# Performance work log

Measured on AMD Instinct MI355X. Metric: run time of the kernel, lower is better.

## Reference

```python
import jax, jax.numpy as jnp
import numpy as np

BETA = 0.1
EPS_LOW = 0.2
EPS_HIGH = 0.2
TEMPERATURE = 1.0
H, V = 1024, 32000
B, T = 4, 1024


def _per_token_logps(hidden, weight, ids):
    # hidden: [B,T,H], weight: [V,H], ids: [B,T] -> gathered log-softmax logps [B,T]
    logits = jnp.einsum('bth,vh->btv', hidden, weight) / TEMPERATURE  # [B,T,V]
    lse = jax.nn.logsumexp(logits, axis=-1)                            # [B,T]
    sel = jnp.take_along_axis(logits, ids[..., None], axis=-1)[..., 0]
    return sel - lse


def setup_inputs() -> dict:
    key = jax.random.key(0)
    k1, k2, k3, k4, k5, k6 = jax.random.split(key, 6)
    x = jax.random.normal(k1, (B, T, H), dtype=jnp.float32)
    ref_input = jax.random.normal(k2, (B, T, H), dtype=jnp.float32)
    # lm-head weights (policy and frozen reference), scaled like nn.Linear init
    weight = jax.random.normal(k3, (V, H), dtype=jnp.float32) * (1.0 / np.sqrt(H))
    ref_weight = jax.random.normal(k4, (V, H), dtype=jnp.float32) * (1.0 / np.sqrt(H))
    selected_token_ids = jax.random.randint(k5, (B, T), 0, V, dtype=jnp.int32)
    attention_mask = jnp.ones((B, T), dtype=jnp.int32)
    advantages = jax.random.normal(k6, (B,), dtype=jnp.float32)
    return {
        'x': x,
        'weight': weight,
        'ref_input': ref_input,
        'ref_weight': ref_weight,
        'advantages': advantages,
        'selected_token_ids': selected_token_ids,
        'attention_mask': attention_mask,
    }


def reference(x, weight, ref_input, ref_weight, advantages, selected_token_ids, attention_mask):
    # policy per-token logps
    logps = _per_token_logps(x, weight, selected_token_ids)  # [B,T]
    # reference model logps (no grad path in original)
    ref_logps = jax.lax.stop_gradient(
        _per_token_logps(ref_input, ref_weight, selected_token_ids))
    # old logps default: detached current logps -> ratio = 1 in forward
    old_logps = jax.lax.stop_gradient(logps)

    log_ratio = logps - old_logps
    coef_1 = jnp.exp(log_ratio)
    coef_2 = jnp.clip(coef_1, 1.0 - EPS_LOW, 1.0 + EPS_HIGH)
    adv = advantages[:, None]  # [B,1]
    per_token_loss = -jnp.minimum(coef_1 * adv, coef_2 * adv)

    # KL penalty to reference model: exp(ref-cur) - (ref-cur) - 1
    d = ref_logps - logps
    kl = jnp.exp(d) - d - 1.0
    per_token_loss = per_token_loss + BETA * kl

    mask = attention_mask.astype(per_token_loss.dtype)
    # loss_type 'bnpo': batch-normalized policy optimization
    loss = jnp.sum(per_token_loss * mask) / jnp.maximum(jnp.sum(mask), 1.0)
    return loss
```

## Files before the change

kernel.cpp:

```cpp
#include <hip/hip_runtime.h>
#include <hip/hip_bf16.h>
#include <math.h>

constexpr int kH   = 1024;
constexpr int kV   = 32000;
constexpr int kTok = 4096;
constexpr int BM   = 256;
constexpr int BN   = 256;
constexpr int BK   = 64;
constexpr int NT   = kH / BK;
constexpr int NVT  = kV / BN;
constexpr int NMT  = kTok / BM;

typedef _Float16 f16x8  __attribute__((ext_vector_type(8)));
typedef float    f32x16 __attribute__((ext_vector_type(16)));

typedef __attribute__((address_space(1))) const void gvoid_t;
typedef __attribute__((address_space(3))) void lvoid_t;

__global__ __launch_bounds__(256) void convert_kernel(
    const float* __restrict__ src, _Float16* __restrict__ dst)
{
  int idx = blockIdx.x * 256 + threadIdx.x;
  int row = idx >> 7;
  int blk = idx & 127;
  int chunk = blk >> 3;
  int c = blk & 7;
  int p = c ^ (row & 7);
  const float* s = src + ((size_t)row << 10) + (blk << 3);
  float4 v0 = *(const float4*)s;
  float4 v1 = *(const float4*)(s + 4);
  f16x8 o = { (_Float16)v0.x, (_Float16)v0.y, (_Float16)v0.z, (_Float16)v0.w,
              (_Float16)v1.x, (_Float16)v1.y, (_Float16)v1.z, (_Float16)v1.w };
  *(f16x8*)&dst[((size_t)row << 10) + (chunk << 6) + (p << 3)] = o;
}

__global__ __launch_bounds__(512, 2) void lse_gemm_kernel(
    const _Float16* __restrict__ X0, const _Float16* __restrict__ W0,
    const _Float16* __restrict__ X1, const _Float16* __restrict__ W1,
    float2* __restrict__ P0, float2* __restrict__ P1)
{
  __shared__ _Float16 lds[2][2][BM * BK];

  const _Float16* Xp = blockIdx.z ? X1 : X0;
  const _Float16* Wp = blockIdx.z ? W1 : W0;
  float2* Pp = blockIdx.z ? P1 : P0;

  const int tid  = threadIdx.x;
  const int wave = tid >> 6;
  const int lane = tid & 63;
  const int l31  = lane & 31;
  const int h    = lane >> 5;
  const int ll7  = lane & 7;
  const int wr   = wave >> 2;
  const int wc   = wave & 3;
  const int srow = lane >> 3;
  const int sblk = lane & 7;

  const int m_base = blockIdx.x * BM;
  const int v_base = blockIdx.y * BN;

  const _Float16* gA = Xp + (size_t)(m_base + wave * 8 + srow) * kH + sblk * 8;
  const _Float16* gB = Wp + (size_t)(v_base + wave * 8 + srow) * kH + sblk * 8;

  const int baseA = (wr * 128 + l31) * BK;
  const int baseV = (wc * 64  + l31) * BK;
  int offK[4];
#pragma unroll
  for (int s = 0; s < 4; ++s) offK[s] = (((s * 2 + h) ^ ll7) << 3);

  f32x16 acc[2][4];
#pragma unroll
  for (int j = 0; j < 2; ++j)
#pragma unroll
    for (int i = 0; i < 4; ++i)
#pragma unroll
      for (int r = 0; r < 16; ++r) acc[j][i][r] = 0.f;

  f16x8 vf[2][4];
  f16x8 tfa[4], tfb[4];

#define STG_A(c, kt, hh) do {                                                       \
    __builtin_amdgcn_global_load_lds(                                               \
        (gvoid_t*)(gA + (size_t)((hh) * 128     ) * kH + (kt) * BK),                \
        (lvoid_t*)&lds[c][0][(((hh) * 128     ) + wave * 8) * BK], 16, 0, 0);       \
    __builtin_amdgcn_global_load_lds(                                               \
        (gvoid_t*)(gA + (size_t)((hh) * 128 + 64) * kH + (kt) * BK),                \
        (lvoid_t*)&lds[c][0][(((hh) * 128 + 64) + wave * 8) * BK], 16, 0, 0);       \
  } while (0)
#define STG_B(c, kt, hh) do {                                                       \
    __builtin_amdgcn_global_load_lds(                                               \
        (gvoid_t*)(gB + (size_t)((hh) * 128     ) * kH + (kt) * BK),                \
        (lvoid_t*)&lds[c][1][(((hh) * 128     ) + wave * 8) * BK], 16, 0, 0);       \
    __builtin_amdgcn_global_load_lds(                                               \
        (gvoid_t*)(gB + (size_t)((hh) * 128 + 64) * kH + (kt) * BK),                \
        (lvoid_t*)&lds[c][1][(((hh) * 128 + 64) + wave * 8) * BK], 16, 0, 0);       \
  } while (0)

#define BAR do { asm volatile("" ::: "memory");                                     \
                 __builtin_amdgcn_s_barrier();                                      \
                 asm volatile("" ::: "memory"); } while (0)
#define VM6  asm volatile("s_waitcnt vmcnt(6)" ::: "memory")
#define VM0  asm volatile("s_waitcnt vmcnt(0)" ::: "memory")

#define RDTF(dst, c, f) do {                                                        \
    _Pragma("unroll")                                                               \
    for (int s = 0; s < 4; ++s)                                                     \
      dst[s] = *(const f16x8*)&lds[c][0][baseA + (f) * 2048 + offK[s]];             \
  } while (0)
#define RDVF(c) do {                                                                \
    _Pragma("unroll")                                                               \
    for (int j = 0; j < 2; ++j)                                                     \
      _Pragma("unroll")                                                             \
      for (int s = 0; s < 4; ++s)                                                   \
        vf[j][s] = *(const f16x8*)&lds[c][1][baseV + j * 2048 + offK[s]];           \
  } while (0)

#define MM(g, TF) do {                                                              \
    __builtin_amdgcn_s_setprio(1);                                                  \
    _Pragma("unroll")                                                               \
    for (int s = 0; s < 4; ++s) {                                                   \
      acc[0][g] = __builtin_amdgcn_mfma_f32_32x32x16_f16(vf[0][s], TF[s], acc[0][g], 0, 0, 0); \
      acc[1][g] = __builtin_amdgcn_mfma_f32_32x32x16_f16(vf[1][s], TF[s], acc[1][g], 0, 0, 0); \
    }                                                                               \
    __builtin_amdgcn_s_setprio(0);                                                  \
  } while (0)

  STG_B(0, 0, 0); STG_B(0, 0, 1); STG_A(0, 0, 0); STG_A(0, 0, 1);
  STG_B(1, 1, 0); STG_B(1, 1, 1); STG_A(1, 1, 0);
  VM6;
  BAR;
  RDVF(0);
  RDTF(tfa, 0, 0);

  for (int kt = 0; kt < NT - 2; kt += 2) {
    STG_A(1, kt + 1, 1); BAR; RDTF(tfb, 0, 1); MM(0, tfa); BAR;
    STG_B(0, kt + 2, 0); BAR; RDTF(tfa, 0, 2); MM(1, tfb); BAR;
    STG_B(0, kt + 2, 1); BAR; RDTF(tfb, 0, 3); MM(2, tfa); BAR;
    STG_A(0, kt + 2, 0); VM6; BAR; RDTF(tfa, 1, 0); MM(3, tfb); RDVF(1); BAR;
    STG_A(0, kt + 2, 1); BAR; RDTF(tfb, 1, 1); MM(0, tfa); BAR;
    STG_B(1, kt + 3, 0); BAR; RDTF(tfa, 1, 2); MM(1, tfb); BAR;
    STG_B(1, kt + 3, 1); BAR; RDTF(tfb, 1, 3); MM(2, tfa); BAR;
    STG_A(1, kt + 3, 0); VM6; BAR; RDTF(tfa, 0, 0); MM(3, tfb); RDVF(0); BAR;
  }

  STG_A(1, NT - 1, 1); BAR; RDTF(tfb, 0, 1); MM(0, tfa); BAR;
  BAR;                      RDTF(tfa, 0, 2); MM(1, tfb); BAR;
  BAR;                      RDTF(tfb, 0, 3); MM(2, tfa); BAR;
  VM0; BAR;                 RDTF(tfa, 1, 0); MM(3, tfb); RDVF(1); BAR;
  BAR;                      RDTF(tfb, 1, 1); MM(0, tfa); BAR;
  BAR;                      RDTF(tfa, 1, 2); MM(1, tfb); BAR;
  BAR;                      RDTF(tfb, 1, 3); MM(2, tfa); BAR;
  BAR;                                       MM(3, tfb);

#undef STG_A
#undef STG_B
#undef RDTF
#undef RDVF
#undef MM

  float* redm = (float*)&lds[0][0][0];
  float* reds = redm + 4 * 256;

#pragma unroll
  for (int i = 0; i < 4; ++i) {
    float m = acc[0][i][0];
#pragma unroll
    for (int r = 1; r < 16; ++r) m = fmaxf(m, acc[0][i][r]);
#pragma unroll
    for (int r = 0; r < 16; ++r) m = fmaxf(m, acc[1][i][r]);
    float s = 0.f;
#pragma unroll
    for (int r = 0; r < 16; ++r) s += __expf(acc[0][i][r] - m);
#pragma unroll
    for (int r = 0; r < 16; ++r) s += __expf(acc[1][i][r] - m);
    float om = __shfl_xor(m, 32, 64);
    float os = __shfl_xor(s, 32, 64);
    float nm = fmaxf(m, om);
    s = s * __expf(m - nm) + os * __expf(om - nm);
    m = nm;
    if (lane < 32) {
      redm[wc * 256 + wr * 128 + i * 32 + lane] = m;
      reds[wc * 256 + wr * 128 + i * 32 + lane] = s;
    }
  }
  __syncthreads();
  if (tid < 256) {
    float M = redm[tid], S = reds[tid];
#pragma unroll
    for (int w = 1; w < 4; ++w) {
      float m2 = redm[w * 256 + tid], s2 = reds[w * 256 + tid];
      float nm = fmaxf(M, m2);
      S = S * __expf(M - nm) + s2 * __expf(m2 - nm);
      M = nm;
    }
    Pp[(size_t)blockIdx.y * kTok + m_base + tid] = make_float2(M, S);
  }
}

__global__ __launch_bounds__(256) void sel_kernel(
    const float* __restrict__ X0, const float* __restrict__ W0,
    const float* __restrict__ X1, const float* __restrict__ W1,
    const int* __restrict__ ids, float* __restrict__ sel0, float* __restrict__ sel1)
{
  const int model = blockIdx.y;
  const float* X = model ? X1 : X0;
  const float* W = model ? W1 : W0;
  float* out = model ? sel1 : sel0;
  const int wave = threadIdx.x >> 6, lane = threadIdx.x & 63;
  const int t  = blockIdx.x * 4 + wave;
  const int id = ids[t];
  const float* xr = X + (size_t)t * kH;
  const float* wr = W + (size_t)id * kH;
  float s = 0.f;
#pragma unroll
  for (int r = 0; r < 4; ++r) {
    int idx = r * 256 + lane * 4;
    float4 a = *(const float4*)&xr[idx];
    float4 b = *(const float4*)&wr[idx];
    s += a.x * b.x + a.y * b.y + a.z * b.z + a.w * b.w;
  }
#pragma unroll
  for (int st = 32; st; st >>= 1) s += __shfl_xor(s, st, 64);
  if (lane == 0) out[t] = s;
}

__global__ __launch_bounds__(256) void finalize_kernel(
    const float2* __restrict__ P0, const float2* __restrict__ P1,
    const float* __restrict__ sel0, const float* __restrict__ sel1,
    const float* __restrict__ adv, const int* __restrict__ mask,
    float* __restrict__ accum)
{
  const int t = blockIdx.x * 256 + threadIdx.x;
  float M0 = -INFINITY, S0 = 0.f, M1 = -INFINITY, S1 = 0.f;
  for (int i = 0; i < NVT; ++i) {
    float2 p = P0[(size_t)i * kTok + t];
    if (p.x > M0) { S0 = S0 * __expf(M0 - p.x) + p.y; M0 = p.x; }
    else          { S0 += p.y * __expf(p.x - M0); }
  }
  for (int i = 0; i < NVT; ++i) {
    float2 p = P1[(size_t)i * kTok + t];
    if (p.x > M1) { S1 = S1 * __expf(M1 - p.x) + p.y; M1 = p.x; }
    else          { S1 += p.y * __expf(p.x - M1); }
  }
  float lse0  = M0 + logf(S0);
  float lse1  = M1 + logf(S1);
  float logp  = sel0[t] - lse0;
  float rlogp = sel1[t] - lse1;
  float d  = rlogp - logp;
  float kl = __expf(d) - d - 1.f;
  float a  = adv[t >> 10];
  float mv = (float)mask[t];
  float loss = (-a + 0.1f * kl) * mv;

#pragma unroll
  for (int st = 32; st; st >>= 1) {
    loss += __shfl_xor(loss, st, 64);
    mv   += __shfl_xor(mv, st, 64);
  }
  __shared__ float lsum[4], msum[4];
  const int wave = threadIdx.x >> 6, lane = threadIdx.x & 63;
  if (lane == 0) { lsum[wave] = loss; msum[wave] = mv; }
  __syncthreads();
  if (threadIdx.x == 0) {
    atomicAdd(&accum[0], lsum[0] + lsum[1] + lsum[2] + lsum[3]);
    atomicAdd(&accum[1], msum[0] + msum[1] + msum[2] + msum[3]);
  }
}

__global__ void scalar_kernel(const float* __restrict__ accum, float* __restrict__ out)
{
  out[0] = accum[0] / fmaxf(accum[1], 1.f);
}

extern "C" void kernel_launch(void* const* d_in, const int* in_sizes, int n_in,
                              void* d_out, int out_size, void* d_ws, size_t ws_size,
                              hipStream_t stream)
{
  const float* x    = (const float*)d_in[0];
  const float* w    = (const float*)d_in[1];
  const float* rx   = (const float*)d_in[2];
  const float* rw   = (const float*)d_in[3];
  const float* adv  = (const float*)d_in[4];
  const int*   ids  = (const int*)d_in[5];
  const int*   mask = (const int*)d_in[6];
  float* out = (float*)d_out;

  char* ws = (char*)d_ws;
  _Float16* Xh  = (_Float16*)ws;
  _Float16* Wh  = Xh + (size_t)kTok * kH;
  _Float16* RXh = Wh + (size_t)kV * kH;
  _Float16* RWh = RXh + (size_t)kTok * kH;
  float2*   P0  = (float2*)(RWh + (size_t)kV * kH);
  float2*   P1  = P0 + (size_t)NVT * kTok;
  float*    sel0 = (float*)(P1 + (size_t)NVT * kTok);
  float*    sel1 = sel0 + kTok;
  float*    accum = sel1 + kTok;

  hipMemsetAsync(accum, 0, 2 * sizeof(float), stream);

  convert_kernel<<<kTok * 128 / 256, 256, 0, stream>>>(x,  Xh);
  convert_kernel<<<kV   * 128 / 256, 256, 0, stream>>>(w,  Wh);
  convert_kernel<<<kTok * 128 / 256, 256, 0, stream>>>(rx, RXh);
  convert_kernel<<<kV   * 128 / 256, 256, 0, stream>>>(rw, RWh);

  sel_kernel<<<dim3(kTok / 4, 2), 256, 0, stream>>>(x, w, rx, rw, ids, sel0, sel1);

  lse_gemm_kernel<<<dim3(NMT, NVT, 2), 512, 0, stream>>>(Xh, Wh, RXh, RWh, P0, P1);

  finalize_kernel<<<kTok / 256, 256, 0, stream>>>(P0, P1, sel0, sel1, adv, mask, accum);
  scalar_kernel<<<1, 1, 0, stream>>>(accum, out);
}
```

Baseline: 916.4 us.

## Pre-pack weights into MFMA fragment layout and load them directly to registers

The weight matrices are now converted into a layout already arranged as per-lane MFMA operand fragments, so the GEMM reads W straight from global memory into registers instead of staging it through LDS. LDS now holds only the X tile, which halves shared-memory use and the ds_read traffic, and the elaborate barrier-interleaved schedule is replaced by a simpler double-buffered loop with two syncthreads per pair of K steps. The cost is that W fragments go through L2/global loads per wave with no LDS reuse across waves in a block, and the coarser synchronisation offers less latency hiding.

```diff
diff --git a/kernel.cpp b/kernel.cpp
--- a/kernel.cpp
+++ b/kernel.cpp
@@ -18,7 +18,7 @@
 typedef __attribute__((address_space(1))) const void gvoid_t;
 typedef __attribute__((address_space(3))) void lvoid_t;
 
-__global__ __launch_bounds__(256) void convert_kernel(
+__global__ __launch_bounds__(256) void convert_x_kernel(
     const float* __restrict__ src, _Float16* __restrict__ dst)
 {
   int idx = blockIdx.x * 256 + threadIdx.x;
@@ -35,12 +35,29 @@
   *(f16x8*)&dst[((size_t)row << 10) + (chunk << 6) + (p << 3)] = o;
 }
 
+__global__ __launch_bounds__(256) void convert_w_kernel(
+    const float* __restrict__ src, _Float16* __restrict__ dst)
+{
+  int t    = blockIdx.x * 256 + threadIdx.x;
+  int lane = t & 63;
+  int s    = (t >> 6) & 63;
+  int vg   = t >> 12;
+  int row  = vg * 32 + (lane & 31);
+  int k0   = s * 16 + (lane >> 5) * 8;
+  const float* p = src + (size_t)row * kH + k0;
+  float4 v0 = *(const float4*)p;
+  float4 v1 = *(const float4*)(p + 4);
+  f16x8 o = { (_Float16)v0.x, (_Float16)v0.y, (_Float16)v0.z, (_Float16)v0.w,
+              (_Float16)v1.x, (_Float16)v1.y, (_Float16)v1.z, (_Float16)v1.w };
+  *(f16x8*)&dst[(size_t)t * 8] = o;
+}
+
 __global__ __launch_bounds__(512, 2) void lse_gemm_kernel(
     const _Float16* __restrict__ X0, const _Float16* __restrict__ W0,
     const _Float16* __restrict__ X1, const _Float16* __restrict__ W1,
     float2* __restrict__ P0, float2* __restrict__ P1)
 {
-  __shared__ _Float16 lds[2][2][BM * BK];
+  __shared__ _Float16 Xs[2][BM * BK];
 
   const _Float16* Xp = blockIdx.z ? X1 : X0;
   const _Float16* Wp = blockIdx.z ? W1 : W0;
@@ -58,13 +75,12 @@
   const int sblk = lane & 7;
 
   const int m_base = blockIdx.x * BM;
-  const int v_base = blockIdx.y * BN;
-
-  const _Float16* gA = Xp + (size_t)(m_base + wave * 8 + srow) * kH + sblk * 8;
-  const _Float16* gB = Wp + (size_t)(v_base + wave * 8 + srow) * kH + sblk * 8;
-
-  const int baseA = (wr * 128 + l31) * BK;
-  const int baseV = (wc * 64  + l31) * BK;
+
+  const _Float16* gX = Xp + (size_t)(m_base + wave * 8 + srow) * kH + sblk * 8;
+  const _Float16* gW = Wp + (size_t)(blockIdx.y * 8 + wc * 2) * 32768
+                          + (size_t)lane * 8;
+
+  const int baseT = (wr * 128 + l31) * BK;
   int offK[4];
 #pragma unroll
   for (int s = 0; s < 4; ++s) offK[s] = (((s * 2 + h) ^ ll7) << 3);
@@ -77,89 +93,67 @@
 #pragma unroll
       for (int r = 0; r < 16; ++r) acc[j][i][r] = 0.f;
 
-  f16x8 vf[2][4];
+  f16x8 vfA[2][4], vfB[2][4];
   f16x8 tfa[4], tfb[4];
 
-#define STG_A(c, kt, hh) do {                                                       \
-    __builtin_amdgcn_global_load_lds(                                               \
-        (gvoid_t*)(gA + (size_t)((hh) * 128     ) * kH + (kt) * BK),                \
-        (lvoid_t*)&lds[c][0][(((hh) * 128     ) + wave * 8) * BK], 16, 0, 0);       \
-    __builtin_amdgcn_global_load_lds(                                               \
-        (gvoid_t*)(gA + (size_t)((hh) * 128 + 64) * kH + (kt) * BK),                \
-        (lvoid_t*)&lds[c][0][(((hh) * 128 + 64) + wave * 8) * BK], 16, 0, 0);       \
-  } while (0)
-#define STG_B(c, kt, hh) do {                                                       \
-    __builtin_amdgcn_global_load_lds(                                               \
-        (gvoid_t*)(gB + (size_t)((hh) * 128     ) * kH + (kt) * BK),                \
-        (lvoid_t*)&lds[c][1][(((hh) * 128     ) + wave * 8) * BK], 16, 0, 0);       \
-    __builtin_amdgcn_global_load_lds(                                               \
-        (gvoid_t*)(gB + (size_t)((hh) * 128 + 64) * kH + (kt) * BK),                \
-        (lvoid_t*)&lds[c][1][(((hh) * 128 + 64) + wave * 8) * BK], 16, 0, 0);       \
-  } while (0)
-
-#define BAR do { asm volatile("" ::: "memory");                                     \
-                 __builtin_amdgcn_s_barrier();                                      \
-                 asm volatile("" ::: "memory"); } while (0)
-#define VM6  asm volatile("s_waitcnt vmcnt(6)" ::: "memory")
-#define VM0  asm volatile("s_waitcnt vmcnt(0)" ::: "memory")
-
-#define RDTF(dst, c, f) do {                                                        \
+#define STG(c, kt) do {                                                             \
     _Pragma("unroll")                                                               \
-    for (int s = 0; s < 4; ++s)                                                     \
-      dst[s] = *(const f16x8*)&lds[c][0][baseA + (f) * 2048 + offK[s]];             \
-  } while (0)
-#define RDVF(c) do {                                                                \
+    for (int i = 0; i < 4; ++i)                                                     \
+      __builtin_amdgcn_global_load_lds(                                             \
+          (gvoid_t*)(gX + (size_t)(i * 64) * kH + (kt) * 64),                       \
+          (lvoid_t*)&Xs[c][(i * 64 + wave * 8) * 64], 16, 0, 0);                    \
+  } while (0)
+
+#define RDW(vf, kt) do {                                                            \
     _Pragma("unroll")                                                               \
     for (int j = 0; j < 2; ++j)                                                     \
       _Pragma("unroll")                                                             \
-      for (int s = 0; s < 4; ++s)                                                   \
-        vf[j][s] = *(const f16x8*)&lds[c][1][baseV + j * 2048 + offK[s]];           \
-  } while (0)
-
-#define MM(g, TF) do {                                                              \
+      for (int ss = 0; ss < 4; ++ss)                                                \
+        vf[j][ss] = *(const f16x8*)(gW + (size_t)(j * 64 + (kt) * 4 + ss) * 512);   \
+  } while (0)
+
+#define RDTF(tf, c, f) do {                                                         \
+    _Pragma("unroll")                                                               \
+    for (int ss = 0; ss < 4; ++ss)                                                  \
+      tf[ss] = *(const f16x8*)&Xs[c][baseT + (f) * 32 * BK + offK[ss]];             \
+  } while (0)
+
+#define MM(g, TF, VF) do {                                                          \
     __builtin_amdgcn_s_setprio(1);                                                  \
     _Pragma("unroll")                                                               \
-    for (int s = 0; s < 4; ++s) {                                                   \
-      acc[0][g] = __builtin_amdgcn_mfma_f32_32x32x16_f16(vf[0][s], TF[s], acc[0][g], 0, 0, 0); \
-      acc[1][g] = __builtin_amdgcn_mfma_f32_32x32x16_f16(vf[1][s], TF[s], acc[1][g], 0, 0, 0); \
+    for (int ss = 0; ss < 4; ++ss) {                                                \
+      acc[0][g] = __builtin_amdgcn_mfma_f32_32x32x16_f16(VF[0][ss], TF[ss], acc[0][g], 0, 0, 0); \
+      acc[1][g] = __builtin_amdgcn_mfma_f32_32x32x16_f16(VF[1][ss], TF[ss], acc[1][g], 0, 0, 0); \
     }                                                                               \
     __builtin_amdgcn_s_setprio(0);                                                  \
   } while (0)
 
-  STG_B(0, 0, 0); STG_B(0, 0, 1); STG_A(0, 0, 0); STG_A(0, 0, 1);
-  STG_B(1, 1, 0); STG_B(1, 1, 1); STG_A(1, 1, 0);
-  VM6;
-  BAR;
-  RDVF(0);
-  RDTF(tfa, 0, 0);
-
-  for (int kt = 0; kt < NT - 2; kt += 2) {
-    STG_A(1, kt + 1, 1); BAR; RDTF(tfb, 0, 1); MM(0, tfa); BAR;
-    STG_B(0, kt + 2, 0); BAR; RDTF(tfa, 0, 2); MM(1, tfb); BAR;
-    STG_B(0, kt + 2, 1); BAR; RDTF(tfb, 0, 3); MM(2, tfa); BAR;
-    STG_A(0, kt + 2, 0); VM6; BAR; RDTF(tfa, 1, 0); MM(3, tfb); RDVF(1); BAR;
-    STG_A(0, kt + 2, 1); BAR; RDTF(tfb, 1, 1); MM(0, tfa); BAR;
-    STG_B(1, kt + 3, 0); BAR; RDTF(tfa, 1, 2); MM(1, tfb); BAR;
-    STG_B(1, kt + 3, 1); BAR; RDTF(tfb, 1, 3); MM(2, tfa); BAR;
-    STG_A(1, kt + 3, 0); VM6; BAR; RDTF(tfa, 0, 0); MM(3, tfb); RDVF(0); BAR;
-  }
-
-  STG_A(1, NT - 1, 1); BAR; RDTF(tfb, 0, 1); MM(0, tfa); BAR;
-  BAR;                      RDTF(tfa, 0, 2); MM(1, tfb); BAR;
-  BAR;                      RDTF(tfb, 0, 3); MM(2, tfa); BAR;
-  VM0; BAR;                 RDTF(tfa, 1, 0); MM(3, tfb); RDVF(1); BAR;
-  BAR;                      RDTF(tfb, 1, 1); MM(0, tfa); BAR;
-  BAR;                      RDTF(tfa, 1, 2); MM(1, tfb); BAR;
-  BAR;                      RDTF(tfb, 1, 3); MM(2, tfa); BAR;
-  BAR;                                       MM(3, tfb);
-
-#undef STG_A
-#undef STG_B
+#define COMPUTE(c, VF) do {                                                         \
+    RDTF(tfa, c, 0); RDTF(tfb, c, 1);                                               \
+    MM(0, tfa, VF);  RDTF(tfa, c, 2);                                               \
+    MM(1, tfb, VF);  RDTF(tfb, c, 3);                                               \
+    MM(2, tfa, VF);  MM(3, tfb, VF);                                                \
+  } while (0)
+
+  STG(0, 0); RDW(vfA, 0);
+  __syncthreads();
+
+  for (int kt = 0; kt < NT; kt += 2) {
+    STG(1, kt + 1); RDW(vfB, kt + 1);
+    COMPUTE(0, vfA);
+    __syncthreads();
+    if (kt < NT - 2) { STG(0, kt + 2); RDW(vfA, kt + 2); }
+    COMPUTE(1, vfB);
+    __syncthreads();
+  }
+
+#undef STG
+#undef RDW
 #undef RDTF
-#undef RDVF
 #undef MM
-
-  float* redm = (float*)&lds[0][0][0];
+#undef COMPUTE
+
+  float* redm = (float*)&Xs[0][0];
   float* reds = redm + 4 * 256;
 
 #pragma unroll
@@ -288,10 +282,10 @@
 
   char* ws = (char*)d_ws;
   _Float16* Xh  = (_Float16*)ws;
-  _Float16* Wh  = Xh + (size_t)kTok * kH;
-  _Float16* RXh = Wh + (size_t)kV * kH;
-  _Float16* RWh = RXh + (size_t)kTok * kH;
-  float2*   P0  = (float2*)(RWh + (size_t)kV * kH);
+  _Float16* Wf  = Xh + (size_t)kTok * kH;
+  _Float16* RXh = Wf + (size_t)kV * kH;
+  _Float16* RWf = RXh + (size_t)kTok * kH;
+  float2*   P0  = (float2*)(RWf + (size_t)kV * kH);
   float2*   P1  = P0 + (size_t)NVT * kTok;
   float*    sel0 = (float*)(P1 + (size_t)NVT * kTok);
   float*    sel1 = sel0 + kTok;
@@ -299,14 +293,14 @@
 
   hipMemsetAsync(accum, 0, 2 * sizeof(float), stream);
 
-  convert_kernel<<<kTok * 128 / 256, 256, 0, stream>>>(x,  Xh);
-  convert_kernel<<<kV   * 128 / 256, 256, 0, stream>>>(w,  Wh);
-  convert_kernel<<<kTok * 128 / 256, 256, 0, stream>>>(rx, RXh);
-  convert_kernel<<<kV   * 128 / 256, 256, 0, stream>>>(rw, RWh);
+  convert_x_kernel<<<kTok * 128 / 256, 256, 0, stream>>>(x,  Xh);
+  convert_x_kernel<<<kTok * 128 / 256, 256, 0, stream>>>(rx, RXh);
+  convert_w_kernel<<<kV / 32 * 64 * 64 / 256, 256, 0, stream>>>(w,  Wf);
+  convert_w_kernel<<<kV / 32 * 64 * 64 / 256, 256, 0, stream>>>(rw, RWf);
 
   sel_kernel<<<dim3(kTok / 4, 2), 256, 0, stream>>>(x, w, rx, rw, ids, sel0, sel1);
 
-  lse_gemm_kernel<<<dim3(NMT, NVT, 2), 512, 0, stream>>>(Xh, Wh, RXh, RWh, P0, P1);
+  lse_gemm_kernel<<<dim3(NMT, NVT, 2), 512, 0, stream>>>(Xh, Wf, RXh, RWf, P0, P1);
 
   finalize_kernel<<<kTok / 256, 256, 0, stream>>>(P0, P1, sel0, sel1, adv, mask, accum);
   scalar_kernel<<<1, 1, 0, stream>>>(accum, out);
```

Measured after the change: 946.1 us. 1.03x slower.
